# Optimization experiments

Measured on AMD Instinct MI355X. Metric: run time of the kernel, lower is better.

Reference implementation:

```python
import jax, jax.numpy as jnp
import numpy as np

# hyperparameters (from init_kwargs)
A_LOG = 1.0
B_LOG = 1.0
C_LOG = 1.0
THR = 0.5
DT = 1.0
EPS = 1e-5


@jax.custom_vjp
def spike(v_scaled):
    # Heaviside forward, fast-sigmoid surrogate backward
    return (v_scaled > 0).astype(jnp.float32)

def _spike_fwd(v_scaled):
    return spike(v_scaled), v_scaled

def _spike_bwd(v_scaled, dy):
    return (dy / (1.0 + 100.0 * jnp.abs(v_scaled)) ** 2,)

spike.defvjp(_spike_fwd, _spike_bwd)


def setup_inputs() -> dict:
    key = jax.random.key(0)
    k1, k2, k3 = jax.random.split(key, 3)
    T, B, N_IN, N_REC = 1000, 128, 256, 256
    x = jax.random.normal(k1, (T, B, N_IN), dtype=jnp.float32)
    z0 = jnp.zeros((B, N_REC), dtype=jnp.float32)
    v0 = jnp.zeros((B, N_REC), dtype=jnp.float32)
    t0 = jnp.zeros((B, N_REC), dtype=jnp.float32)
    # RandomNormal(stddev=0.01) init for input weights
    w_in = 0.01 * jax.random.normal(k2, (N_IN, N_REC), dtype=jnp.float32)
    # recurrence enabled: small random recurrent weights
    w_rec = 0.01 * jax.random.normal(k3, (N_REC, N_REC), dtype=jnp.float32)
    return {"x": x, "z0": z0, "v0": v0, "t0": t0, "w_in": w_in, "w_rec": w_rec}


def _step(carry, x_t, w_in, w_rec):
    z, v, t = carry                              # each [B, n_rec]
    i_in = x_t @ w_in + z @ w_rec                # [B, n_rec]
    h = (i_in != 0).astype(jnp.float32)          # activity flag
    new_t = t + (1.0 - h)                        # (h != 1) == 1 - h since h in {0,1}
    new_v = v * (1.0 - z)                        # reset on spike
    low_pass = (new_v > -1.0).astype(jnp.float32)
    new_v = new_v - (1.0 - low_pass) * (new_v + 1.0)   # clamp at -1
    # logarithmic leak
    cap = (jnp.exp2(jnp.abs(new_v) / C_LOG) - B_LOG) / A_LOG
    arg = jnp.minimum(DT * h * (new_t + 1.0), cap)
    new_v = new_v - jnp.sign(new_v) * C_LOG * jnp.log2(EPS + A_LOG * arg + B_LOG)
    new_v = new_v + i_in
    new_t = new_t * (1.0 - h)
    new_z = spike((new_v - THR) / THR)
    return (new_z, new_v, new_t), (new_z, new_v)


def reference(x, z0, v0, t0, w_in, w_rec):
    def step(carry, x_t):
        return _step(carry, x_t, w_in, w_rec)
    _, (zs, vs) = jax.lax.scan(step, (z0, v0, t0), x)
    return zs, vs  # each [T, B, n_rec]
```

## Files before the change

kernel.cpp:

```cpp
#include <hip/hip_runtime.h>

__global__ __launch_bounds__(256) void gemm_xw(const float* __restrict__ X,
                                               const float* __restrict__ W,
                                               float* __restrict__ Y,
                                               int M) {
    __shared__ float As[32][132];
    __shared__ float Bs[32][128];

    const int tid = threadIdx.x;
    const int mb = blockIdx.x >> 1;
    const int nb = blockIdx.x & 1;
    const int m0 = mb << 7;
    const int n0 = nb << 7;
    const int tr = (tid >> 4) << 3;
    const int tc = (tid & 15) << 3;

    float acc[8][8];
#pragma unroll
    for (int i = 0; i < 8; ++i)
#pragma unroll
        for (int j = 0; j < 8; ++j) acc[i][j] = 0.f;

    for (int kb = 0; kb < 256; kb += 32) {
#pragma unroll
        for (int i = 0; i < 4; ++i) {
            int f = tid + (i << 8);
            int row = f >> 3, kq = f & 7;
            float4 a = *(const float4*)(X + (size_t)(m0 + row) * 256 + kb + (kq << 2));
            As[(kq << 2) + 0][row] = a.x;
            As[(kq << 2) + 1][row] = a.y;
            As[(kq << 2) + 2][row] = a.z;
            As[(kq << 2) + 3][row] = a.w;
            int rowb = f >> 5, cq = f & 31;
            *(float4*)&Bs[rowb][cq << 2] =
                *(const float4*)(W + (size_t)(kb + rowb) * 256 + n0 + (cq << 2));
        }
        __syncthreads();
#pragma unroll
        for (int k = 0; k < 32; ++k) {
            float a[8], b[8];
            *(float4*)&a[0] = *(const float4*)&As[k][tr];
            *(float4*)&a[4] = *(const float4*)&As[k][tr + 4];
            *(float4*)&b[0] = *(const float4*)&Bs[k][tc];
            *(float4*)&b[4] = *(const float4*)&Bs[k][tc + 4];
#pragma unroll
            for (int i = 0; i < 8; ++i)
#pragma unroll
                for (int j = 0; j < 8; ++j)
                    acc[i][j] = fmaf(a[i], b[j], acc[i][j]);
        }
        __syncthreads();
    }
#pragma unroll
    for (int i = 0; i < 8; ++i) {
        float* yp = Y + (size_t)(m0 + tr + i) * 256 + n0 + tc;
        *(float4*)yp = make_float4(acc[i][0], acc[i][1], acc[i][2], acc[i][3]);
        *(float4*)(yp + 4) = make_float4(acc[i][4], acc[i][5], acc[i][6], acc[i][7]);
    }
}

__global__ __launch_bounds__(256) void lif_seq4(const float* __restrict__ ix,
                                                const float* __restrict__ wrec,
                                                const float* __restrict__ z0,
                                                const float* __restrict__ v0,
                                                const float* __restrict__ t0,
                                                float* __restrict__ zs,
                                                float* __restrict__ vs,
                                                int T, int B) {
    const int b = blockIdx.x;
    const int tid = threadIdx.x;
    const int wv = tid >> 6;
    const int lane = tid & 63;
    const size_t sb = (size_t)b * 256 + tid;
    const size_t stride = (size_t)B * 256;

    __shared__ unsigned long long smask[2][4];

    float v = v0[sb];
    float t = t0[sb];
    bool sp = (z0[sb] != 0.f);
    int p = 0;

    const float* ixp = ix + sb;

    constexpr float G0 = 1e-5f + 1.0f;

    auto step = [&](float rr, float& zo_, float& vo_) {
        unsigned long long mk = __ballot(sp);
        if (lane == 0) smask[p][wv] = mk;
        __syncthreads();
        unsigned long long m0 = smask[p][0];
        unsigned long long m1 = smask[p][1];
        unsigned long long m2 = smask[p][2];
        unsigned long long m3 = smask[p][3];
        p ^= 1;

        float vc = fmaxf(sp ? 0.f : v, -1.f);
        float E  = __builtin_amdgcn_exp2f(fabsf(vc));
        float cA = (1e-5f + (E - 1.f)) + 1.f;
        float tp1 = t + 1.f;
        bool hz = (rr == 0.f);
        float cT = hz ? G0 : ((1e-5f + tp1) + 1.f);
        float L  = __builtin_amdgcn_logf(fminf(cT, cA));
        float Ls = copysignf(L, vc);
        float nvp = (vc == 0.f) ? vc : (vc - Ls);
        float nv  = nvp + rr;
        float ntn = hz ? tp1 : 0.f;

        if ((m0 | m1 | m2 | m3) != 0ull) {
            float ir = 0.f;
            unsigned long long mm;
            mm = m0;
            while (mm) { int j = __builtin_ctzll(mm); mm &= mm - 1;
                ir += wrec[((size_t)j << 8) + tid]; }
            mm = m1;
            while (mm) { int j = __builtin_ctzll(mm); mm &= mm - 1;
                ir += wrec[((size_t)(64 + j) << 8) + tid]; }
            mm = m2;
            while (mm) { int j = __builtin_ctzll(mm); mm &= mm - 1;
                ir += wrec[((size_t)(128 + j) << 8) + tid]; }
            mm = m3;
            while (mm) { int j = __builtin_ctzll(mm); mm &= mm - 1;
                ir += wrec[((size_t)(192 + j) << 8) + tid]; }

            float i_in = rr + ir;
            bool hz2 = (i_in == 0.f);
            float cT2 = hz2 ? G0 : ((1e-5f + tp1) + 1.f);
            float L2  = __builtin_amdgcn_logf(fminf(cT2, cA));
            float Ls2 = copysignf(L2, vc);
            float nvp2 = (vc == 0.f) ? vc : (vc - Ls2);
            nv  = nvp2 + i_in;
            ntn = hz2 ? tp1 : 0.f;
        }

        sp = (nv > 0.5f);
        v = nv;
        t = ntn;
        zo_ = sp ? 1.f : 0.f;
        vo_ = nv;
    };

    float iA[4], iB[4], zo[4], vo[4];

    auto loadChunk = [&](float (&bf)[4], int c0) {
#pragma unroll
        for (int u = 0; u < 4; ++u) {
            int r = c0 + u;
            r = (r < T) ? r : T - 1;
            bf[u] = ixp[(size_t)r * stride];
        }
    };

    auto runChunk = [&](float (&bf)[4], int c0) {
#pragma unroll
        for (int u = 0; u < 4; ++u) step(bf[u], zo[u], vo[u]);
#pragma unroll
        for (int u = 0; u < 4; ++u) {
            size_t o = (size_t)(c0 + u) * stride + sb;
            zs[o] = zo[u];
            vs[o] = vo[u];
        }
    };

    loadChunk(iA, 0);
    int c = 0;
    while (c + 8 <= T) {
        loadChunk(iB, c + 4);
        runChunk(iA, c);
        loadChunk(iA, c + 8);
        runChunk(iB, c + 4);
        c += 8;
    }
    if (c + 4 <= T) {
        runChunk(iA, c);
        c += 4;
    }
    for (int ts = c; ts < T; ++ts) {
        float r = ixp[(size_t)ts * stride];
        float zz, vv;
        step(r, zz, vv);
        size_t o = (size_t)ts * stride + sb;
        zs[o] = zz;
        vs[o] = vv;
    }
}

extern "C" void kernel_launch(void* const* d_in, const int* in_sizes, int n_in,
                              void* d_out, int out_size, void* d_ws, size_t ws_size,
                              hipStream_t stream) {
    const float* x    = (const float*)d_in[0];
    const float* z0   = (const float*)d_in[1];
    const float* v0   = (const float*)d_in[2];
    const float* t0   = (const float*)d_in[3];
    const float* w_in = (const float*)d_in[4];
    const float* wrec = (const float*)d_in[5];

    const int n_rec = 256;
    const int B = in_sizes[1] / n_rec;
    const int nin = in_sizes[4] / n_rec;
    const int T = in_sizes[0] / (B * nin);
    const int M = T * B;

    float* zs = (float*)d_out;
    float* vs = zs + (size_t)T * B * n_rec;
    float* ixbuf = zs;

    gemm_xw<<<dim3((M / 128) * 2), dim3(256), 0, stream>>>(x, w_in, ixbuf, M);
    lif_seq4<<<dim3(B), dim3(256), 0, stream>>>(ixbuf, wrec, z0, v0, t0, zs, vs, T, B);
}
```

Baseline: 498.9 us.

## Fuse input GEMM and LIF scan into one kernel with per-chunk flag sync

Merges the input-projection GEMM and the sequential LIF recurrence into a single launch. The first B blocks run the scan at raised priority, and the remaining blocks compute GEMM tiles and release per-timestep-chunk atomic counters. Scan blocks spin on acquire loads of these counters before reading each chunk, so the GEMM overlaps with the serial recurrence instead of running before it. The cost is a memset of the flags plus spin-wait polling. It also relies on the scan blocks and GEMM blocks being co-resident, so that GEMM blocks are not starved while scan blocks spin.

Result: slower. 1.433 ms (+187.3%).

```diff
diff --git a/kernel.cpp b/kernel.cpp
--- a/kernel.cpp
+++ b/kernel.cpp
@@ -1,89 +1,103 @@
 #include <hip/hip_runtime.h>
 
-__global__ __launch_bounds__(256) void gemm_xw(const float* __restrict__ X,
-                                               const float* __restrict__ W,
-                                               float* __restrict__ Y,
-                                               int M) {
+__global__ __launch_bounds__(256) void lif_fused(const float* __restrict__ X,
+                                                 const float* __restrict__ W,
+                                                 const float* __restrict__ wrec,
+                                                 const float* __restrict__ z0,
+                                                 const float* __restrict__ v0,
+                                                 const float* __restrict__ t0,
+                                                 float* __restrict__ zs,
+                                                 float* __restrict__ vs,
+                                                 int* __restrict__ flags,
+                                                 int T, int B) {
     __shared__ float As[32][132];
     __shared__ float Bs[32][128];
+    __shared__ unsigned long long smask[2][4];
 
     const int tid = threadIdx.x;
-    const int mb = blockIdx.x >> 1;
-    const int nb = blockIdx.x & 1;
-    const int m0 = mb << 7;
-    const int n0 = nb << 7;
-    const int tr = (tid >> 4) << 3;
-    const int tc = (tid & 15) << 3;
-
-    float acc[8][8];
-#pragma unroll
-    for (int i = 0; i < 8; ++i)
-#pragma unroll
-        for (int j = 0; j < 8; ++j) acc[i][j] = 0.f;
-
-    for (int kb = 0; kb < 256; kb += 32) {
-#pragma unroll
-        for (int i = 0; i < 4; ++i) {
-            int f = tid + (i << 8);
-            int row = f >> 3, kq = f & 7;
-            float4 a = *(const float4*)(X + (size_t)(m0 + row) * 256 + kb + (kq << 2));
-            As[(kq << 2) + 0][row] = a.x;
-            As[(kq << 2) + 1][row] = a.y;
-            As[(kq << 2) + 2][row] = a.z;
-            As[(kq << 2) + 3][row] = a.w;
-            int rowb = f >> 5, cq = f & 31;
-            *(float4*)&Bs[rowb][cq << 2] =
-                *(const float4*)(W + (size_t)(kb + rowb) * 256 + n0 + (cq << 2));
-        }
-        __syncthreads();
-#pragma unroll
-        for (int k = 0; k < 32; ++k) {
-            float a[8], b[8];
-            *(float4*)&a[0] = *(const float4*)&As[k][tr];
-            *(float4*)&a[4] = *(const float4*)&As[k][tr + 4];
-            *(float4*)&b[0] = *(const float4*)&Bs[k][tc];
-            *(float4*)&b[4] = *(const float4*)&Bs[k][tc + 4];
-#pragma unroll
-            for (int i = 0; i < 8; ++i)
-#pragma unroll
-                for (int j = 0; j < 8; ++j)
-                    acc[i][j] = fmaf(a[i], b[j], acc[i][j]);
-        }
-        __syncthreads();
-    }
-#pragma unroll
-    for (int i = 0; i < 8; ++i) {
-        float* yp = Y + (size_t)(m0 + tr + i) * 256 + n0 + tc;
-        *(float4*)yp = make_float4(acc[i][0], acc[i][1], acc[i][2], acc[i][3]);
-        *(float4*)(yp + 4) = make_float4(acc[i][4], acc[i][5], acc[i][6], acc[i][7]);
-    }
-}
-
-__global__ __launch_bounds__(256) void lif_seq4(const float* __restrict__ ix,
-                                                const float* __restrict__ wrec,
-                                                const float* __restrict__ z0,
-                                                const float* __restrict__ v0,
-                                                const float* __restrict__ t0,
-                                                float* __restrict__ zs,
-                                                float* __restrict__ vs,
-                                                int T, int B) {
+
+    if ((int)blockIdx.x >= B) {
+        const int gb = blockIdx.x - B;
+        const int mb = gb >> 1;
+        const int nb = gb & 1;
+        const int m0 = mb << 7;
+        const int n0 = nb << 7;
+        const int tr = (tid >> 4) << 3;
+        const int tc = (tid & 15) << 3;
+
+        float acc[8][8];
+#pragma unroll
+        for (int i = 0; i < 8; ++i)
+#pragma unroll
+            for (int j = 0; j < 8; ++j) acc[i][j] = 0.f;
+
+        for (int kb = 0; kb < 256; kb += 32) {
+#pragma unroll
+            for (int i = 0; i < 4; ++i) {
+                int f = tid + (i << 8);
+                int row = f >> 3, kq = f & 7;
+                float4 a = *(const float4*)(X + (size_t)(m0 + row) * 256 + kb + (kq << 2));
+                As[(kq << 2) + 0][row] = a.x;
+                As[(kq << 2) + 1][row] = a.y;
+                As[(kq << 2) + 2][row] = a.z;
+                As[(kq << 2) + 3][row] = a.w;
+                int rowb = f >> 5, cq = f & 31;
+                *(float4*)&Bs[rowb][cq << 2] =
+                    *(const float4*)(W + (size_t)(kb + rowb) * 256 + n0 + (cq << 2));
+            }
+            __syncthreads();
+#pragma unroll
+            for (int k = 0; k < 32; ++k) {
+                float a[8], bb[8];
+                *(float4*)&a[0] = *(const float4*)&As[k][tr];
+                *(float4*)&a[4] = *(const float4*)&As[k][tr + 4];
+                *(float4*)&bb[0] = *(const float4*)&Bs[k][tc];
+                *(float4*)&bb[4] = *(const float4*)&Bs[k][tc + 4];
+#pragma unroll
+                for (int i = 0; i < 8; ++i)
+#pragma unroll
+                    for (int j = 0; j < 8; ++j)
+                        acc[i][j] = fmaf(a[i], bb[j], acc[i][j]);
+            }
+            __syncthreads();
+        }
+#pragma unroll
+        for (int i = 0; i < 8; ++i) {
+            float* yp = zs + (size_t)(m0 + tr + i) * 256 + n0 + tc;
+            *(float4*)yp = make_float4(acc[i][0], acc[i][1], acc[i][2], acc[i][3]);
+            *(float4*)(yp + 4) = make_float4(acc[i][4], acc[i][5], acc[i][6], acc[i][7]);
+        }
+        if ((tid & 63) == 0)
+            __hip_atomic_fetch_add(&flags[mb >> 2], 1, __ATOMIC_RELEASE,
+                                   __HIP_MEMORY_SCOPE_AGENT);
+        return;
+    }
+
+    __builtin_amdgcn_s_setprio(3);
+
     const int b = blockIdx.x;
-    const int tid = threadIdx.x;
     const int wv = tid >> 6;
     const int lane = tid & 63;
     const size_t sb = (size_t)b * 256 + tid;
     const size_t stride = (size_t)B * 256;
 
-    __shared__ unsigned long long smask[2][4];
-
     float v = v0[sb];
     float t = t0[sb];
     bool sp = (z0[sb] != 0.f);
     int p = 0;
 
-    const float* ixp = ix + sb;
+    const float* ixp = zs + sb;
 
     constexpr float G0 = 1e-5f + 1.0f;
+
+    auto waitChunk = [&](int c0) {
+        int k = ((c0 < T) ? c0 : (T - 1)) >> 2;
+        int hi = 4 * (k + 1); if (hi > T) hi = T;
+        int need = 8 * (hi - 4 * k);
+        while (__hip_atomic_load(&flags[k], __ATOMIC_ACQUIRE,
+                                 __HIP_MEMORY_SCOPE_AGENT) < need)
+            __builtin_amdgcn_s_sleep(32);
+    };
 
     auto step = [&](float rr, float& zo_, float& vo_) {
         unsigned long long mk = __ballot(sp);
@@ -162,11 +176,14 @@
         }
     };
 
+    waitChunk(0);
     loadChunk(iA, 0);
     int c = 0;
     while (c + 8 <= T) {
+        waitChunk(c + 4);
         loadChunk(iB, c + 4);
         runChunk(iA, c);
+        waitChunk(c + 8);
         loadChunk(iA, c + 8);
         runChunk(iB, c + 4);
         c += 8;
@@ -176,6 +193,7 @@
         c += 4;
     }
     for (int ts = c; ts < T; ++ts) {
+        waitChunk(ts);
         float r = ixp[(size_t)ts * stride];
         float zz, vv;
         step(r, zz, vv);
@@ -203,8 +221,12 @@
 
     float* zs = (float*)d_out;
     float* vs = zs + (size_t)T * B * n_rec;
-    float* ixbuf = zs;
-
-    gemm_xw<<<dim3((M / 128) * 2), dim3(256), 0, stream>>>(x, w_in, ixbuf, M);
-    lif_seq4<<<dim3(B), dim3(256), 0, stream>>>(ixbuf, wrec, z0, v0, t0, zs, vs, T, B);
+    int* flags = (int*)d_ws;
+    const int nflags = (T + 3) / 4;
+
+    hipMemsetAsync(flags, 0, (size_t)nflags * sizeof(int), stream);
+
+    const int gemmBlocks = (M / 128) * 2;
+    lif_fused<<<dim3(B + gemmBlocks), dim3(256), 0, stream>>>(
+        x, w_in, wrec, z0, v0, t0, zs, vs, flags, T, B);
 }
```
